# Kernel tuning notes

Measured on AMD Instinct MI355X. Metric: run time of the kernel, lower is better.

## Reference

```python
import jax, jax.numpy as jnp
import numpy as np
import math

L, R, B, S, D = 103, 512, 2, 512, 768


def setup_inputs() -> dict:
    key = jax.random.key(0)
    ks = jax.random.split(key, 16)
    n = lambda k, sh, s=1.0: jax.random.normal(k, sh, jnp.float32) * s
    W = 0.02  # weight init scale keeps softmax logits well-conditioned
    return {
        "output": n(ks[0], (B, S, D)),              # BERT sequence output (backbone treated as feature extractor)
        "attention_mask": jnp.ones((B, S), jnp.int32),
        "laws": n(ks[1], (L, R, D)),                # precomputed law representations (laws_rep.pkl)
        "Wq": n(ks[2], (D, D), W), "bq": jnp.zeros((D,), jnp.float32),
        "Wk": n(ks[3], (D, D), W), "bk": jnp.zeros((D,), jnp.float32),
        "Wv": n(ks[4], (D, D), W), "bv": jnp.zeros((D,), jnp.float32),
        "w_law_d": n(ks[5], (D,), W), "b_law_d": jnp.zeros((1,), jnp.float32),
        "w_law1": n(ks[6], (R,), W), "b_law1": jnp.zeros((1,), jnp.float32),
        "w_accu_d": n(ks[7], (D,), W), "b_accu_d": jnp.zeros((1,), jnp.float32),
        "w_accu1": n(ks[8], (R,), W), "b_accu1": jnp.zeros((1,), jnp.float32),
        "W_accu2": n(ks[9], (119, L), W), "b_accu2": jnp.zeros((119,), jnp.float32),
        "w_term_d": n(ks[10], (D,), W), "b_term_d": jnp.zeros((1,), jnp.float32),
        "w_term1": n(ks[11], (R,), W), "b_term1": jnp.zeros((1,), jnp.float32),
        "W_term2": n(ks[12], (11, L), W), "b_term2": jnp.zeros((11,), jnp.float32),
    }


def _forward(output, mask_f, laws, Wq, bq, Wk, bk, Wv, bv,
             w_law_d, b_law_d, w_law1, b_law1,
             w_accu_d, b_accu_d, w_accu1, b_accu1, W_accu2, b_accu2,
             w_term_d, b_term_d, w_term1, b_term1, W_term2, b_term2):
    laws_q = laws @ Wq + bq          # [L,R,D]
    facts_k = output @ Wk + bk       # [B,S,D]
    facts_v = output @ Wv + bv       # [B,S,D]
    # relevance: [L,B,R,S]
    scores = jnp.einsum('lrd,bsd->lbrs', laws_q, facts_k) / math.sqrt(768)
    scores = scores + (1.0 - mask_f)[None, :, None, :] * -10000.0
    probs = jax.nn.softmax(scores, axis=-1)          # (dropout omitted: eval mode)
    a_facts = jnp.einsum('lbrs,bsd->lbrd', probs, facts_v)
    g = jnp.transpose(a_facts, (1, 0, 2, 3))         # [B,L,R,D]
    act = jnp.tanh
    # law head: law1(tanh(law_d(g)))  -> [B,L]
    law = act(jnp.einsum('blrd,d->blr', g, w_law_d) + b_law_d)
    law = jnp.einsum('blr,r->bl', law, w_law1) + b_law1
    # accu head: accu2(tanh(accu1(tanh(accu_d(g))))) -> [B,119]
    accu = act(jnp.einsum('blrd,d->blr', g, w_accu_d) + b_accu_d)
    accu = act(jnp.einsum('blr,r->bl', accu, w_accu1) + b_accu1)
    accu = accu @ W_accu2.T + b_accu2
    # term head -> [B,11]
    term = act(jnp.einsum('blrd,d->blr', g, w_term_d) + b_term_d)
    term = act(jnp.einsum('blr,r->bl', term, w_term1) + b_term1)
    term = term @ W_term2.T + b_term2
    return law, accu, term


def reference(output, attention_mask, laws, Wq, bq, Wk, bk, Wv, bv,
              w_law_d, b_law_d, w_law1, b_law1,
              w_accu_d, b_accu_d, w_accu1, b_accu1, W_accu2, b_accu2,
              w_term_d, b_term_d, w_term1, b_term1, W_term2, b_term2):
    mask_f = attention_mask.astype(jnp.float32)
    return _forward(output, mask_f, laws, Wq, bq, Wk, bk, Wv, bv,
                    w_law_d, b_law_d, w_law1, b_law1,
                    w_accu_d, b_accu_d, w_accu1, b_accu1, W_accu2, b_accu2,
                    w_term_d, b_term_d, w_term1, b_term1, W_term2, b_term2)
```

## Files before the change

kernel.cpp:

```cpp
#include <hip/hip_runtime.h>

static constexpr int nL = 103, nR = 512, nB = 2, nS = 512, nD = 768;
static constexpr float INV_SQRT_D = 0.03608439182435161f;

typedef short bf16x8 __attribute__((ext_vector_type(8)));
typedef float f32x4 __attribute__((ext_vector_type(4)));
typedef unsigned short u16;
typedef unsigned short ushort4v __attribute__((ext_vector_type(4)));
typedef unsigned short ushort8v __attribute__((ext_vector_type(8)));

static constexpr size_t OFF_OUTB = 0;
static constexpr size_t OFF_MBF  = 393216;
static constexpr size_t OFF_KQB  = 688128;
static constexpr size_t OFF_QBK  = 1081344;
static constexpr size_t OFF_WKBQ = OFF_QBK + 768;
static constexpr size_t OFF_WV3  = OFF_WKBQ + 768;
static constexpr size_t OFF_CST  = OFF_WV3 + 2304;
static constexpr size_t OFF_C    = OFF_CST + 4;
static constexpr size_t OFF_HV   = OFF_C + 1024;
static constexpr size_t OFF_SUM  = OFF_HV + 3072;

__device__ inline float wredsum(float v) {
#pragma unroll
  for (int o = 32; o; o >>= 1) v += __shfl_xor(v, o);
  return v;
}

__device__ inline u16 f2bf(float f) {
  unsigned u = __builtin_bit_cast(unsigned, f);
  u += 0x7FFFu + ((u >> 16) & 1u);
  return (u16)(u >> 16);
}

__device__ inline bf16x8 cvt8(float4 a, float4 b) {
  ushort8v u;
  u[0]=f2bf(a.x); u[1]=f2bf(a.y); u[2]=f2bf(a.z); u[3]=f2bf(a.w);
  u[4]=f2bf(b.x); u[5]=f2bf(b.y); u[6]=f2bf(b.z); u[7]=f2bf(b.w);
  return __builtin_bit_cast(bf16x8, u);
}

__device__ inline void st4(u16* dst, float4 g) {
  ushort4v u;
  u[0]=f2bf(g.x); u[1]=f2bf(g.y); u[2]=f2bf(g.z); u[3]=f2bf(g.w);
  *(ushort4v*)dst = u;
}

__global__ __launch_bounds__(256) void k_prep_mm(
    const float* __restrict__ Wq, const float* __restrict__ Wk,
    const float* __restrict__ Wv, const float* __restrict__ bq,
    const float* __restrict__ bk, const float* __restrict__ bv,
    const float* __restrict__ wld, const float* __restrict__ wad,
    const float* __restrict__ wtd, const float* __restrict__ outp,
    float* __restrict__ ws) {
  int tid = threadIdx.x, lane = tid & 63, w = tid >> 6;
  int bid = blockIdx.x;
  if (bid < 192) {
    int row = bid * 4 + w;
    const float* wqr = Wq + (size_t)row * nD;
    const float* wkr = Wk + (size_t)row * nD;
    const float* wvr = Wv + (size_t)row * nD;
    float dq = 0.f, dk = 0.f, d0 = 0.f, d1 = 0.f, d2 = 0.f;
#pragma unroll
    for (int k = 0; k < 3; ++k) {
      int off = lane * 4 + k * 256;
      float4 q4 = *(const float4*)(wqr + off);
      float4 k4 = *(const float4*)(wkr + off);
      float4 v4 = *(const float4*)(wvr + off);
      float4 bk4 = *(const float4*)(bk + off);
      float4 bq4 = *(const float4*)(bq + off);
      float4 l4 = *(const float4*)(wld + off);
      float4 a4 = *(const float4*)(wad + off);
      float4 t4 = *(const float4*)(wtd + off);
      dq += q4.x*bk4.x + q4.y*bk4.y + q4.z*bk4.z + q4.w*bk4.w;
      dk += k4.x*bq4.x + k4.y*bq4.y + k4.z*bq4.z + k4.w*bq4.w;
      d0 += v4.x*l4.x + v4.y*l4.y + v4.z*l4.z + v4.w*l4.w;
      d1 += v4.x*a4.x + v4.y*a4.y + v4.z*a4.z + v4.w*a4.w;
      d2 += v4.x*t4.x + v4.y*t4.y + v4.z*t4.z + v4.w*t4.w;
    }
    dq = wredsum(dq); dk = wredsum(dk);
    d0 = wredsum(d0); d1 = wredsum(d1); d2 = wredsum(d2);
    if (lane == 0) {
      ws[OFF_QBK + row] = dq;
      ws[OFF_WKBQ + row] = dk;
      ws[OFF_WV3 + row] = d0;
      ws[OFF_WV3 + 768 + row] = d1;
      ws[OFF_WV3 + 1536 + row] = d2;
    }
  } else if (bid == 192) {
    if (tid < 64) {
      float c0 = 0.f, c1 = 0.f, c2 = 0.f, c3 = 0.f;
      for (int j = lane; j < nD; j += 64) {
        c0 += bq[j]*bk[j]; c1 += bv[j]*wld[j]; c2 += bv[j]*wad[j]; c3 += bv[j]*wtd[j];
      }
      c0 = wredsum(c0); c1 = wredsum(c1); c2 = wredsum(c2); c3 = wredsum(c3);
      if (lane == 0) {
        ws[OFF_CST+0] = c0; ws[OFF_CST+1] = c1; ws[OFF_CST+2] = c2; ws[OFF_CST+3] = c3;
      }
    }
    for (int i = tid; i < 3 * nB * nL; i += 256) ws[OFF_SUM + i] = 0.f;
  } else if (bid < 385) {
    u16* outb = (u16*)(ws + OFF_OUTB);
    size_t e = ((size_t)(bid - 193) * 256 + tid) * 16;
    float4 f0 = *(const float4*)(outp + e);
    float4 f1 = *(const float4*)(outp + e + 4);
    float4 f2 = *(const float4*)(outp + e + 8);
    float4 f3 = *(const float4*)(outp + e + 12);
    *(ushort8v*)(outb + e)     = __builtin_bit_cast(ushort8v, cvt8(f0, f1));
    *(ushort8v*)(outb + e + 8) = __builtin_bit_cast(ushort8v, cvt8(f2, f3));
  } else {
    u16* Mbf = (u16*)(ws + OFF_MBF);
    const int mb = bid - 385;
    const int ti = mb / 12, tj = mb % 12;
    const int c4 = lane & 15, q4 = lane >> 4, wr = w >> 1, wc = w & 1;
    f32x4 acc[2][2];
#pragma unroll
    for (int i = 0; i < 2; ++i)
#pragma unroll
      for (int j = 0; j < 2; ++j) acc[i][j] = (f32x4){0.f,0.f,0.f,0.f};
    const float* Ab[2]; const float* Bb[2];
#pragma unroll
    for (int i = 0; i < 2; ++i)
      Ab[i] = Wq + (size_t)(ti*64 + wr*32 + i*16 + c4) * nD + q4*8;
#pragma unroll
    for (int j = 0; j < 2; ++j)
      Bb[j] = Wk + (size_t)(tj*64 + wc*32 + j*16 + c4) * nD + q4*8;
    for (int kt = 0; kt < 24; ++kt) {
      bf16x8 af[2], bf[2];
#pragma unroll
      for (int i = 0; i < 2; ++i)
        af[i] = cvt8(*(const float4*)(Ab[i] + kt*32), *(const float4*)(Ab[i] + kt*32 + 4));
#pragma unroll
      for (int j = 0; j < 2; ++j)
        bf[j] = cvt8(*(const float4*)(Bb[j] + kt*32), *(const float4*)(Bb[j] + kt*32 + 4));
#pragma unroll
      for (int i = 0; i < 2; ++i)
#pragma unroll
        for (int j = 0; j < 2; ++j)
          acc[i][j] = __builtin_amdgcn_mfma_f32_16x16x32_bf16(af[i], bf[j], acc[i][j], 0, 0, 0);
    }
#pragma unroll
    for (int i = 0; i < 2; ++i)
#pragma unroll
      for (int j = 0; j < 2; ++j) {
        int n = tj*64 + wc*32 + j*16 + c4;
#pragma unroll
        for (int reg = 0; reg < 4; ++reg) {
          int m = ti*64 + wr*32 + i*16 + q4*4 + reg;
          Mbf[(size_t)m * nD + n] = f2bf(acc[i][j][reg]);
        }
      }
  }
}

__global__ __launch_bounds__(256) void k_mkq_chv(
    const float* __restrict__ outp, float* __restrict__ ws) {
  int tid = threadIdx.x, lane = tid & 63, w = tid >> 6;
  int bid = blockIdx.x;
  if (bid < 192) {
    const u16* outb = (const u16*)(ws + OFF_OUTB);
    const u16* Mbf  = (const u16*)(ws + OFF_MBF);
    u16* kqB = (u16*)(ws + OFF_KQB);
    const float* qbk = ws + OFF_QBK;
    const int c4 = lane & 15, q4 = lane >> 4, wr = w >> 1, wc = w & 1;
    const int ti = bid / 12, tj = bid % 12;
    f32x4 acc[2][2];
#pragma unroll
    for (int i = 0; i < 2; ++i)
#pragma unroll
      for (int j = 0; j < 2; ++j) acc[i][j] = (f32x4){0.f,0.f,0.f,0.f};
    const u16* Ab[2]; const u16* Bb[2];
#pragma unroll
    for (int i = 0; i < 2; ++i)
      Ab[i] = outb + (size_t)(ti*64 + wr*32 + i*16 + c4) * nD + q4*8;
#pragma unroll
    for (int j = 0; j < 2; ++j)
      Bb[j] = Mbf + (size_t)(tj*64 + wc*32 + j*16 + c4) * nD + q4*8;
    for (int kt = 0; kt < 24; ++kt) {
      bf16x8 af[2], bf[2];
#pragma unroll
      for (int i = 0; i < 2; ++i) af[i] = *(const bf16x8*)(Ab[i] + kt*32);
#pragma unroll
      for (int j = 0; j < 2; ++j) bf[j] = *(const bf16x8*)(Bb[j] + kt*32);
#pragma unroll
      for (int i = 0; i < 2; ++i)
#pragma unroll
        for (int j = 0; j < 2; ++j)
          acc[i][j] = __builtin_amdgcn_mfma_f32_16x16x32_bf16(af[i], bf[j], acc[i][j], 0, 0, 0);
    }
#pragma unroll
    for (int i = 0; i < 2; ++i)
#pragma unroll
      for (int j = 0; j < 2; ++j) {
        int n = tj*64 + wc*32 + j*16 + c4;
        float bb = qbk[n];
#pragma unroll
        for (int reg = 0; reg < 4; ++reg) {
          int m = ti*64 + wr*32 + i*16 + q4*4 + reg;
          kqB[(((size_t)(n >> 3)) << 13) + ((size_t)m << 3) + (n & 7)] =
              f2bf(acc[i][j][reg] + bb);
        }
      }
  } else {
    int idx = (bid - 192) * 4 + w;
    const float* row = outp + (size_t)idx * nD;
    const float* wkbq = ws + OFF_WKBQ;
    const float* wv0 = ws + OFF_WV3;
    const float* wv1 = ws + OFF_WV3 + 768;
    const float* wv2 = ws + OFF_WV3 + 1536;
    float a0 = 0.f, a1 = 0.f, a2 = 0.f, a3 = 0.f;
#pragma unroll
    for (int k = 0; k < 3; ++k) {
      int off = lane * 4 + k * 256;
      float4 o4 = *(const float4*)(row + off);
      float4 k4 = *(const float4*)(wkbq + off);
      float4 l4 = *(const float4*)(wv0 + off);
      float4 c4v = *(const float4*)(wv1 + off);
      float4 t4 = *(const float4*)(wv2 + off);
      a0 += o4.x*k4.x + o4.y*k4.y + o4.z*k4.z + o4.w*k4.w;
      a1 += o4.x*l4.x + o4.y*l4.y + o4.z*l4.z + o4.w*l4.w;
      a2 += o4.x*c4v.x + o4.y*c4v.y + o4.z*c4v.z + o4.w*c4v.w;
      a3 += o4.x*t4.x + o4.y*t4.y + o4.z*t4.z + o4.w*t4.w;
    }
    a0 = wredsum(a0); a1 = wredsum(a1); a2 = wredsum(a2); a3 = wredsum(a3);
    if (lane == 0) {
      ws[OFF_C + idx]         = a0 + ws[OFF_CST+0];
      ws[OFF_HV + idx]        = a1 + ws[OFF_CST+1];
      ws[OFF_HV + 1024 + idx] = a2 + ws[OFF_CST+2];
      ws[OFF_HV + 2048 + idx] = a3 + ws[OFF_CST+3];
    }
  }
}

__global__ __launch_bounds__(512, 4) void k_attn(
    const float* __restrict__ laws, const u16* __restrict__ kqB,
    const int* __restrict__ mask, float* __restrict__ ws,
    const float* __restrict__ bld, const float* __restrict__ wl1,
    const float* __restrict__ bad, const float* __restrict__ wa1,
    const float* __restrict__ btd, const float* __restrict__ wt1) {
  __shared__ u16 Abuf[2][64 * 200];
  __shared__ f32x4 redS[8][64];
  const int tid = threadIdx.x, lane = tid & 63, w = tid >> 6;
  const int c4 = lane & 15, q4 = lane >> 4;
  const int b = blockIdx.x, rt8 = blockIdx.y, l = blockIdx.z;

  const int sr = tid >> 3, sq = tid & 7;
  const float* Asrc = laws + ((size_t)l * nR + rt8 * 64 + sr) * nD + sq * 4;
  const int awo = sr * 200 + sq * 4;

  const u16* Bbase = kqB + ((size_t)q4 * 1024 + (size_t)b * nS + w * 64 + c4) * 8;

  f32x4 acc[4][4];
#pragma unroll
  for (int rt = 0; rt < 4; ++rt)
#pragma unroll
    for (int ct = 0; ct < 4; ++ct) acc[rt][ct] = (f32x4){0.f,0.f,0.f,0.f};

#pragma unroll
  for (int j = 0; j < 3; ++j) {
    float4 p0 = *(const float4*)(Asrc + (2*j) * 32);
    float4 p1 = *(const float4*)(Asrc + (2*j+1) * 32);
    st4(&Abuf[0][0] + awo + (2*j) * 32, p0);
    st4(&Abuf[0][0] + awo + (2*j+1) * 32, p1);
  }
  __syncthreads();

#define COMPUTE_KK(CUR, KT, KK)                                               \
  do {                                                                        \
    bf16x8 bf0 = *(const bf16x8*)(Bbase + (size_t)(KT) * 32768 + 0 * 128);    \
    bf16x8 bf1 = *(const bf16x8*)(Bbase + (size_t)(KT) * 32768 + 1 * 128);    \
    bf16x8 bf2 = *(const bf16x8*)(Bbase + (size_t)(KT) * 32768 + 2 * 128);    \
    bf16x8 bf3 = *(const bf16x8*)(Bbase + (size_t)(KT) * 32768 + 3 * 128);    \
    _Pragma("unroll")                                                         \
    for (int rt = 0; rt < 4; ++rt) {                                          \
      bf16x8 af = *(const bf16x8*)&(CUR)[(rt * 16 + c4) * 200 + (KK) * 32 + q4 * 8]; \
      acc[rt][0] = __builtin_amdgcn_mfma_f32_16x16x32_bf16(af, bf0, acc[rt][0], 0, 0, 0); \
      acc[rt][1] = __builtin_amdgcn_mfma_f32_16x16x32_bf16(af, bf1, acc[rt][1], 0, 0, 0); \
      acc[rt][2] = __builtin_amdgcn_mfma_f32_16x16x32_bf16(af, bf2, acc[rt][2], 0, 0, 0); \
      acc[rt][3] = __builtin_amdgcn_mfma_f32_16x16x32_bf16(af, bf3, acc[rt][3], 0, 0, 0); \
    }                                                                         \
  } while (0)

#pragma unroll
  for (int s = 0; s < 4; ++s) {
    const u16* cur = &Abuf[s & 1][0];
    u16* nxt = &Abuf[(s & 1) ^ 1][0];
    float4 g0, g1;
    if (s < 3) {
      g0 = *(const float4*)(Asrc + (s + 1) * 192 + 0 * 32);
      g1 = *(const float4*)(Asrc + (s + 1) * 192 + 1 * 32);
    }
    COMPUTE_KK(cur, s * 6 + 0, 0);
    COMPUTE_KK(cur, s * 6 + 1, 1);
    if (s < 3) {
      st4(nxt + awo + 0 * 32, g0);
      st4(nxt + awo + 1 * 32, g1);
      g0 = *(const float4*)(Asrc + (s + 1) * 192 + 2 * 32);
      g1 = *(const float4*)(Asrc + (s + 1) * 192 + 3 * 32);
    }
    COMPUTE_KK(cur, s * 6 + 2, 2);
    COMPUTE_KK(cur, s * 6 + 3, 3);
    if (s < 3) {
      st4(nxt + awo + 2 * 32, g0);
      st4(nxt + awo + 3 * 32, g1);
      g0 = *(const float4*)(Asrc + (s + 1) * 192 + 4 * 32);
      g1 = *(const float4*)(Asrc + (s + 1) * 192 + 5 * 32);
    }
    COMPUTE_KK(cur, s * 6 + 4, 4);
    COMPUTE_KK(cur, s * 6 + 5, 5);
    if (s < 3) {
      st4(nxt + awo + 4 * 32, g0);
      st4(nxt + awo + 5 * 32, g1);
    }
    __syncthreads();
  }
#undef COMPUTE_KK

  const float* cp  = ws + OFF_C + (size_t)b * nS;
  const float* hlp = ws + OFF_HV + (size_t)b * nS;
  const float* hap = ws + OFF_HV + 1024 + (size_t)b * nS;
  const float* htp = ws + OFF_HV + 2048 + (size_t)b * nS;
  float cc[4], hl[4], ha[4], ht[4], ma[4];
#pragma unroll
  for (int ct = 0; ct < 4; ++ct) {
    int s = w * 64 + ct * 16 + c4;
    cc[ct] = cp[s]; hl[ct] = hlp[s]; ha[ct] = hap[s]; ht[ct] = htp[s];
    ma[ct] = (1.0f - (float)mask[b * nS + s]) * -10000.0f;
  }

#pragma unroll
  for (int rt = 0; rt < 4; ++rt) {
#pragma unroll
    for (int reg = 0; reg < 4; ++reg) {
      float sse = 0.f, spl = 0.f, spa = 0.f, spt = 0.f;
#pragma unroll
      for (int ct = 0; ct < 4; ++ct) {
        float x = (acc[rt][ct][reg] + cc[ct]) * INV_SQRT_D + ma[ct];
        float e = __expf(x);
        sse += e; spl += e * hl[ct]; spa += e * ha[ct]; spt += e * ht[ct];
      }
#pragma unroll
      for (int o = 1; o < 16; o <<= 1) {
        sse += __shfl_xor(sse, o);
        spl += __shfl_xor(spl, o);
        spa += __shfl_xor(spa, o);
        spt += __shfl_xor(spt, o);
      }
      if (c4 == 0)
        redS[w][rt * 16 + q4 * 4 + reg] = (f32x4){sse, spl, spa, spt};
    }
  }
  __syncthreads();

  if (w == 0) {
    int row = lane;
    f32x4 t = (f32x4){0.f,0.f,0.f,0.f};
#pragma unroll
    for (int wc = 0; wc < 8; ++wc) t += redS[wc][row];
    float inv = 1.0f / t[0];
    int r = rt8 * 64 + row;
    float cl = tanhf(t[1] * inv + bld[0]) * wl1[r];
    float ca = tanhf(t[2] * inv + bad[0]) * wa1[r];
    float ctv = tanhf(t[3] * inv + btd[0]) * wt1[r];
#pragma unroll
    for (int o = 1; o < 64; o <<= 1) {
      cl += __shfl_xor(cl, o);
      ca += __shfl_xor(ca, o);
      ctv += __shfl_xor(ctv, o);
    }
    if (lane == 0) {
      float* sums = ws + OFF_SUM;
      atomicAdd(&sums[b * nL + l], cl);
      atomicAdd(&sums[nB * nL + b * nL + l], ca);
      atomicAdd(&sums[2 * nB * nL + b * nL + l], ctv);
    }
  }
}

__global__ void k_final(const float* __restrict__ ws, float* __restrict__ out,
                        const float* __restrict__ bl1, const float* __restrict__ ba1,
                        const float* __restrict__ Wa2, const float* __restrict__ ba2,
                        const float* __restrict__ bt1, const float* __restrict__ Wt2,
                        const float* __restrict__ bt2) {
  __shared__ float abl[nB * nL], tbl[nB * nL];
  int t = threadIdx.x;
  const float* sl = ws + OFF_SUM;
  const float* sa = sl + nB * nL;
  const float* st = sa + nB * nL;
  if (t < nB * nL) {
    out[t] = sl[t] + bl1[0];
    abl[t] = tanhf(sa[t] + ba1[0]);
    tbl[t] = tanhf(st[t] + bt1[0]);
  }
  __syncthreads();
  for (int idx = t; idx < nB * 119; idx += 256) {
    int b = idx / 119, j = idx % 119;
    float a = ba2[j];
    for (int ll = 0; ll < nL; ++ll) a += Wa2[j * nL + ll] * abl[b * nL + ll];
    out[nB * nL + idx] = a;
  }
  for (int idx = t; idx < nB * 11; idx += 256) {
    int b = idx / 11, j = idx % 11;
    float a = bt2[j];
    for (int ll = 0; ll < nL; ++ll) a += Wt2[j * nL + ll] * tbl[b * nL + ll];
    out[nB * nL + nB * 119 + idx] = a;
  }
}

extern "C" void kernel_launch(void* const* d_in, const int* in_sizes, int n_in,
                              void* d_out, int out_size, void* d_ws, size_t ws_size,
                              hipStream_t stream) {
  (void)in_sizes; (void)n_in; (void)out_size; (void)ws_size;
  const float* outp = (const float*)d_in[0];
  const int*   mask = (const int*)d_in[1];
  const float* laws = (const float*)d_in[2];
  const float* Wq = (const float*)d_in[3];  const float* bq = (const float*)d_in[4];
  const float* Wk = (const float*)d_in[5];  const float* bk = (const float*)d_in[6];
  const float* Wv = (const float*)d_in[7];  const float* bv = (const float*)d_in[8];
  const float* wld = (const float*)d_in[9];  const float* bld = (const float*)d_in[10];
  const float* wl1 = (const float*)d_in[11]; const float* bl1 = (const float*)d_in[12];
  const float* wad = (const float*)d_in[13]; const float* bad = (const float*)d_in[14];
  const float* wa1 = (const float*)d_in[15]; const float* ba1 = (const float*)d_in[16];
  const float* Wa2 = (const float*)d_in[17]; const float* ba2 = (const float*)d_in[18];
  const float* wtd = (const float*)d_in[19]; const float* btd = (const float*)d_in[20];
  const float* wt1 = (const float*)d_in[21]; const float* bt1 = (const float*)d_in[22];
  const float* Wt2 = (const float*)d_in[23]; const float* bt2 = (const float*)d_in[24];
  float* ws = (float*)d_ws;
  float* fout = (float*)d_out;
  u16* kqB = (u16*)(ws + OFF_KQB);

  k_prep_mm<<<529, 256, 0, stream>>>(Wq, Wk, Wv, bq, bk, bv, wld, wad, wtd, outp, ws);
  k_mkq_chv<<<448, 256, 0, stream>>>(outp, ws);
  k_attn<<<dim3(nB, 8, nL), 512, 0, stream>>>(laws, kqB, mask, ws,
                                              bld, wl1, bad, wa1, btd, wt1);
  k_final<<<1, 256, 0, stream>>>(ws, fout, bl1, ba1, Wa2, ba2, bt1, Wt2, bt2);
}
```

Before: 412.7 us.

## Split attention key range across blocks, prefetch K tiles in registers, add row finalize kernel

```diff
diff --git a/kernel.cpp b/kernel.cpp
--- a/kernel.cpp
+++ b/kernel.cpp
@@ -19,6 +19,8 @@
 static constexpr size_t OFF_C    = OFF_CST + 4;
 static constexpr size_t OFF_HV   = OFF_C + 1024;
 static constexpr size_t OFF_SUM  = OFF_HV + 3072;
+static constexpr size_t OFF_PS = 0;
+static constexpr size_t PSN = (size_t)nB * nL * nR;
 
 __device__ inline float wredsum(float v) {
 #pragma unroll
@@ -231,23 +233,27 @@
   }
 }
 
-__global__ __launch_bounds__(512, 4) void k_attn(
+__global__ __launch_bounds__(256) void k_zero(float* __restrict__ ws) {
+  size_t i = ((size_t)blockIdx.x * 256 + threadIdx.x) * 4;
+  *(float4*)(ws + OFF_PS + i) = (float4){0.f, 0.f, 0.f, 0.f};
+}
+
+__global__ __launch_bounds__(256, 3) void k_attn(
     const float* __restrict__ laws, const u16* __restrict__ kqB,
-    const int* __restrict__ mask, float* __restrict__ ws,
-    const float* __restrict__ bld, const float* __restrict__ wl1,
-    const float* __restrict__ bad, const float* __restrict__ wa1,
-    const float* __restrict__ btd, const float* __restrict__ wt1) {
+    const int* __restrict__ mask, float* __restrict__ ws) {
   __shared__ u16 Abuf[2][64 * 200];
-  __shared__ f32x4 redS[8][64];
+  f32x4* redS = (f32x4*)&Abuf[0][0];
   const int tid = threadIdx.x, lane = tid & 63, w = tid >> 6;
   const int c4 = lane & 15, q4 = lane >> 4;
-  const int b = blockIdx.x, rt8 = blockIdx.y, l = blockIdx.z;
-
-  const int sr = tid >> 3, sq = tid & 7;
+  const int b = blockIdx.x >> 1, cs = blockIdx.x & 1;
+  const int rt8 = blockIdx.y, l = blockIdx.z;
+
+  const int sr = tid >> 2, sq = tid & 3;
   const float* Asrc = laws + ((size_t)l * nR + rt8 * 64 + sr) * nD + sq * 4;
   const int awo = sr * 200 + sq * 4;
 
-  const u16* Bbase = kqB + ((size_t)q4 * 1024 + (size_t)b * nS + w * 64 + c4) * 8;
+  const u16* Bbase =
+      kqB + ((size_t)q4 * 1024 + (size_t)b * nS + cs * 256 + w * 64 + c4) * 8;
 
   f32x4 acc[4][4];
 #pragma unroll
@@ -257,74 +263,106 @@
 
 #pragma unroll
   for (int j = 0; j < 3; ++j) {
-    float4 p0 = *(const float4*)(Asrc + (2*j) * 32);
-    float4 p1 = *(const float4*)(Asrc + (2*j+1) * 32);
-    st4(&Abuf[0][0] + awo + (2*j) * 32, p0);
-    st4(&Abuf[0][0] + awo + (2*j+1) * 32, p1);
+    float4 t0 = *(const float4*)(Asrc + (4*j + 0) * 16);
+    float4 t1 = *(const float4*)(Asrc + (4*j + 1) * 16);
+    float4 t2 = *(const float4*)(Asrc + (4*j + 2) * 16);
+    float4 t3 = *(const float4*)(Asrc + (4*j + 3) * 16);
+    st4(&Abuf[0][0] + awo + (4*j + 0) * 16, t0);
+    st4(&Abuf[0][0] + awo + (4*j + 1) * 16, t1);
+    st4(&Abuf[0][0] + awo + (4*j + 2) * 16, t2);
+    st4(&Abuf[0][0] + awo + (4*j + 3) * 16, t3);
   }
   __syncthreads();
 
-#define COMPUTE_KK(CUR, KT, KK)                                               \
+#define LOADB(P, KT)                                                          \
   do {                                                                        \
-    bf16x8 bf0 = *(const bf16x8*)(Bbase + (size_t)(KT) * 32768 + 0 * 128);    \
-    bf16x8 bf1 = *(const bf16x8*)(Bbase + (size_t)(KT) * 32768 + 1 * 128);    \
-    bf16x8 bf2 = *(const bf16x8*)(Bbase + (size_t)(KT) * 32768 + 2 * 128);    \
-    bf16x8 bf3 = *(const bf16x8*)(Bbase + (size_t)(KT) * 32768 + 3 * 128);    \
+    P[0] = *(const bf16x8*)(Bbase + (size_t)(KT) * 32768 + 0 * 128);          \
+    P[1] = *(const bf16x8*)(Bbase + (size_t)(KT) * 32768 + 1 * 128);          \
+    P[2] = *(const bf16x8*)(Bbase + (size_t)(KT) * 32768 + 2 * 128);          \
+    P[3] = *(const bf16x8*)(Bbase + (size_t)(KT) * 32768 + 3 * 128);          \
+  } while (0)
+
+#define CONSUME(P, KK)                                                        \
+  do {                                                                        \
     _Pragma("unroll")                                                         \
     for (int rt = 0; rt < 4; ++rt) {                                          \
-      bf16x8 af = *(const bf16x8*)&(CUR)[(rt * 16 + c4) * 200 + (KK) * 32 + q4 * 8]; \
-      acc[rt][0] = __builtin_amdgcn_mfma_f32_16x16x32_bf16(af, bf0, acc[rt][0], 0, 0, 0); \
-      acc[rt][1] = __builtin_amdgcn_mfma_f32_16x16x32_bf16(af, bf1, acc[rt][1], 0, 0, 0); \
-      acc[rt][2] = __builtin_amdgcn_mfma_f32_16x16x32_bf16(af, bf2, acc[rt][2], 0, 0, 0); \
-      acc[rt][3] = __builtin_amdgcn_mfma_f32_16x16x32_bf16(af, bf3, acc[rt][3], 0, 0, 0); \
+      bf16x8 af = *(const bf16x8*)&cur[(rt * 16 + c4) * 200 + (KK) * 32 + q4 * 8]; \
+      acc[rt][0] = __builtin_amdgcn_mfma_f32_16x16x32_bf16(af, P[0], acc[rt][0], 0, 0, 0); \
+      acc[rt][1] = __builtin_amdgcn_mfma_f32_16x16x32_bf16(af, P[1], acc[rt][1], 0, 0, 0); \
+      acc[rt][2] = __builtin_amdgcn_mfma_f32_16x16x32_bf16(af, P[2], acc[rt][2], 0, 0, 0); \
+      acc[rt][3] = __builtin_amdgcn_mfma_f32_16x16x32_bf16(af, P[3], acc[rt][3], 0, 0, 0); \
     }                                                                         \
   } while (0)
+
+  bf16x8 p0[4], p1[4], p2[4];
+  LOADB(p0, 0);
+  LOADB(p1, 1);
 
 #pragma unroll
   for (int s = 0; s < 4; ++s) {
     const u16* cur = &Abuf[s & 1][0];
     u16* nxt = &Abuf[(s & 1) ^ 1][0];
-    float4 g0, g1;
+    const int kt0 = s * 6;
+    float4 g0, g1, g2, g3;
+    LOADB(p2, kt0 + 2);
     if (s < 3) {
-      g0 = *(const float4*)(Asrc + (s + 1) * 192 + 0 * 32);
-      g1 = *(const float4*)(Asrc + (s + 1) * 192 + 1 * 32);
-    }
-    COMPUTE_KK(cur, s * 6 + 0, 0);
-    COMPUTE_KK(cur, s * 6 + 1, 1);
+      g0 = *(const float4*)(Asrc + (s + 1) * 192 + 0 * 16);
+      g1 = *(const float4*)(Asrc + (s + 1) * 192 + 1 * 16);
+      g2 = *(const float4*)(Asrc + (s + 1) * 192 + 2 * 16);
+      g3 = *(const float4*)(Asrc + (s + 1) * 192 + 3 * 16);
+    }
+    CONSUME(p0, 0);
+    LOADB(p0, kt0 + 3);
+    CONSUME(p1, 1);
     if (s < 3) {
-      st4(nxt + awo + 0 * 32, g0);
-      st4(nxt + awo + 1 * 32, g1);
-      g0 = *(const float4*)(Asrc + (s + 1) * 192 + 2 * 32);
-      g1 = *(const float4*)(Asrc + (s + 1) * 192 + 3 * 32);
-    }
-    COMPUTE_KK(cur, s * 6 + 2, 2);
-    COMPUTE_KK(cur, s * 6 + 3, 3);
+      st4(nxt + awo + 0 * 16, g0);
+      st4(nxt + awo + 1 * 16, g1);
+      st4(nxt + awo + 2 * 16, g2);
+      st4(nxt + awo + 3 * 16, g3);
+      g0 = *(const float4*)(Asrc + (s + 1) * 192 + 4 * 16);
+      g1 = *(const float4*)(Asrc + (s + 1) * 192 + 5 * 16);
+      g2 = *(const float4*)(Asrc + (s + 1) * 192 + 6 * 16);
+      g3 = *(const float4*)(Asrc + (s + 1) * 192 + 7 * 16);
+    }
+    LOADB(p1, kt0 + 4);
+    CONSUME(p2, 2);
+    LOADB(p2, kt0 + 5);
+    CONSUME(p0, 3);
     if (s < 3) {
-      st4(nxt + awo + 2 * 32, g0);
-      st4(nxt + awo + 3 * 32, g1);
-      g0 = *(const float4*)(Asrc + (s + 1) * 192 + 4 * 32);
-      g1 = *(const float4*)(Asrc + (s + 1) * 192 + 5 * 32);
-    }
-    COMPUTE_KK(cur, s * 6 + 4, 4);
-    COMPUTE_KK(cur, s * 6 + 5, 5);
+      st4(nxt + awo + 4 * 16, g0);
+      st4(nxt + awo + 5 * 16, g1);
+      st4(nxt + awo + 6 * 16, g2);
+      st4(nxt + awo + 7 * 16, g3);
+      g0 = *(const float4*)(Asrc + (s + 1) * 192 + 8 * 16);
+      g1 = *(const float4*)(Asrc + (s + 1) * 192 + 9 * 16);
+      g2 = *(const float4*)(Asrc + (s + 1) * 192 + 10 * 16);
+      g3 = *(const float4*)(Asrc + (s + 1) * 192 + 11 * 16);
+    }
+    if (kt0 + 6 < 24) LOADB(p0, kt0 + 6);
+    CONSUME(p1, 4);
+    if (kt0 + 7 < 24) LOADB(p1, kt0 + 7);
+    CONSUME(p2, 5);
     if (s < 3) {
-      st4(nxt + awo + 4 * 32, g0);
-      st4(nxt + awo + 5 * 32, g1);
+      st4(nxt + awo + 8 * 16, g0);
+      st4(nxt + awo + 9 * 16, g1);
+      st4(nxt + awo + 10 * 16, g2);
+      st4(nxt + awo + 11 * 16, g3);
     }
     __syncthreads();
   }
-#undef COMPUTE_KK
+#undef LOADB
+#undef CONSUME
 
   const float* cp  = ws + OFF_C + (size_t)b * nS;
   const float* hlp = ws + OFF_HV + (size_t)b * nS;
   const float* hap = ws + OFF_HV + 1024 + (size_t)b * nS;
   const float* htp = ws + OFF_HV + 2048 + (size_t)b * nS;
-  float cc[4], hl[4], ha[4], ht[4], ma[4];
+  float cadd[4], hl[4], ha[4], ht[4];
 #pragma unroll
   for (int ct = 0; ct < 4; ++ct) {
-    int s = w * 64 + ct * 16 + c4;
-    cc[ct] = cp[s]; hl[ct] = hlp[s]; ha[ct] = hap[s]; ht[ct] = htp[s];
-    ma[ct] = (1.0f - (float)mask[b * nS + s]) * -10000.0f;
+    int s = cs * 256 + w * 64 + ct * 16 + c4;
+    cadd[ct] = cp[s] * INV_SQRT_D + (1.0f - (float)mask[b * nS + s]) * -10000.0f;
+    hl[ct] = hlp[s]; ha[ct] = hap[s]; ht[ct] = htp[s];
   }
 
 #pragma unroll
@@ -334,7 +372,7 @@
       float sse = 0.f, spl = 0.f, spa = 0.f, spt = 0.f;
 #pragma unroll
       for (int ct = 0; ct < 4; ++ct) {
-        float x = (acc[rt][ct][reg] + cc[ct]) * INV_SQRT_D + ma[ct];
+        float x = acc[rt][ct][reg] * INV_SQRT_D + cadd[ct];
         float e = __expf(x);
         sse += e; spl += e * hl[ct]; spa += e * ha[ct]; spt += e * ht[ct];
       }
@@ -346,33 +384,51 @@
         spt += __shfl_xor(spt, o);
       }
       if (c4 == 0)
-        redS[w][rt * 16 + q4 * 4 + reg] = (f32x4){sse, spl, spa, spt};
+        redS[w * 64 + rt * 16 + q4 * 4 + reg] = (f32x4){sse, spl, spa, spt};
     }
   }
   __syncthreads();
 
   if (w == 0) {
-    int row = lane;
     f32x4 t = (f32x4){0.f,0.f,0.f,0.f};
 #pragma unroll
-    for (int wc = 0; wc < 8; ++wc) t += redS[wc][row];
-    float inv = 1.0f / t[0];
-    int r = rt8 * 64 + row;
-    float cl = tanhf(t[1] * inv + bld[0]) * wl1[r];
-    float ca = tanhf(t[2] * inv + bad[0]) * wa1[r];
-    float ctv = tanhf(t[3] * inv + btd[0]) * wt1[r];
-#pragma unroll
-    for (int o = 1; o < 64; o <<= 1) {
-      cl += __shfl_xor(cl, o);
-      ca += __shfl_xor(ca, o);
-      ctv += __shfl_xor(ctv, o);
-    }
-    if (lane == 0) {
-      float* sums = ws + OFF_SUM;
-      atomicAdd(&sums[b * nL + l], cl);
-      atomicAdd(&sums[nB * nL + b * nL + l], ca);
-      atomicAdd(&sums[2 * nB * nL + b * nL + l], ctv);
-    }
+    for (int wc = 0; wc < 4; ++wc) t += redS[wc * 64 + lane];
+    size_t idx = ((size_t)(b * nL + l)) * nR + rt8 * 64 + lane;
+    float* PS = ws + OFF_PS;
+    atomicAdd(&PS[idx], t[0]);
+    atomicAdd(&PS[PSN + idx], t[1]);
+    atomicAdd(&PS[2 * PSN + idx], t[2]);
+    atomicAdd(&PS[3 * PSN + idx], t[3]);
+  }
+}
+
+__global__ __launch_bounds__(512) void k_rowfin(
+    float* __restrict__ ws,
+    const float* __restrict__ bld, const float* __restrict__ wl1,
+    const float* __restrict__ bad, const float* __restrict__ wa1,
+    const float* __restrict__ btd, const float* __restrict__ wt1) {
+  __shared__ float red[3][8];
+  const int x = blockIdx.x;
+  const int b = x / nL, l = x % nL;
+  const int tid = threadIdx.x, lane = tid & 63, w = tid >> 6;
+  const int r = tid;
+  const float* PS = ws + OFF_PS;
+  size_t idx = ((size_t)(b * nL + l)) * nR + r;
+  float inv = 1.0f / PS[idx];
+  float cl = tanhf(PS[PSN + idx] * inv + bld[0]) * wl1[r];
+  float ca = tanhf(PS[2 * PSN + idx] * inv + bad[0]) * wa1[r];
+  float ct = tanhf(PS[3 * PSN + idx] * inv + btd[0]) * wt1[r];
+  cl = wredsum(cl); ca = wredsum(ca); ct = wredsum(ct);
+  if (lane == 0) { red[0][w] = cl; red[1][w] = ca; red[2][w] = ct; }
+  __syncthreads();
+  if (tid == 0) {
+    float a0 = 0.f, a1 = 0.f, a2 = 0.f;
+#pragma unroll
+    for (int i = 0; i < 8; ++i) { a0 += red[0][i]; a1 += red[1][i]; a2 += red[2][i]; }
+    float* sums = ws + OFF_SUM;
+    sums[b * nL + l] = a0;
+    sums[nB * nL + b * nL + l] = a1;
+    sums[2 * nB * nL + b * nL + l] = a2;
   }
 }
 
@@ -430,7 +486,8 @@
 
   k_prep_mm<<<529, 256, 0, stream>>>(Wq, Wk, Wv, bq, bk, bv, wld, wad, wtd, outp, ws);
   k_mkq_chv<<<448, 256, 0, stream>>>(outp, ws);
-  k_attn<<<dim3(nB, 8, nL), 512, 0, stream>>>(laws, kqB, mask, ws,
-                                              bld, wl1, bad, wa1, btd, wt1);
+  k_zero<<<412, 256, 0, stream>>>(ws);
+  k_attn<<<dim3(4, 8, nL), 256, 0, stream>>>(laws, kqB, mask, ws);
+  k_rowfin<<<nB * nL, 512, 0, stream>>>(ws, bld, wl1, bad, wa1, btd, wt1);
   k_final<<<1, 256, 0, stream>>>(ws, fout, bl1, ba1, Wa2, ba2, bt1, Wt2, bt2);
 }
```

After: 448.8 us. +8.8%, slower.
